# Kernel optimization log

Measured on AMD Instinct MI355X. Metric: run time of the kernel, lower is better.

The kernel has to match this reference:

```python
import jax, jax.numpy as jnp
import numpy as np

BLOCK = 32          # MX block size along the contraction dim
E4M3_MAX = 448.0    # max finite magnitude of float8_e4m3fn
E4M3_MAX_EXP = 8.0  # floor(log2(448)) = 8


def mxfp8_quant_dequant(t):
    """Simulate MXFP8 (OCP MX spec): per-32-block E8M0 power-of-two scale,
    elements cast to float8_e4m3fn, then dequantized back to fp32."""
    orig_shape = t.shape
    tb = t.reshape(-1, BLOCK)
    amax = jnp.max(jnp.abs(tb), axis=-1, keepdims=True)
    # E8M0 shared scale: 2^(floor(log2(amax)) - emax_e4m3)
    exp = jnp.floor(jnp.log2(jnp.maximum(amax, 2.0 ** -126))) - E4M3_MAX_EXP
    scale = jnp.exp2(exp)
    q = jnp.clip(tb / scale, -E4M3_MAX, E4M3_MAX)
    q = q.astype(jnp.float8_e4m3fn).astype(t.dtype)  # round-to-nearest fp8
    return (q * scale).reshape(orig_shape)


def setup_inputs() -> dict:
    key = jax.random.key(0)
    k1, k2, k3 = jax.random.split(key, 3)
    B, S, D_IN, D_OUT = 4, 4096, 4096, 4096
    x = jax.random.normal(k1, (B, S, D_IN), dtype=jnp.float32)
    weight = jax.random.normal(k2, (D_OUT, D_IN), dtype=jnp.float32) * 0.02
    bias = jax.random.normal(k3, (D_OUT,), dtype=jnp.float32) * 0.02
    return {"x": x, "weight": weight, "bias": bias}


def reference(x, weight, bias):
    B, S, D_IN = x.shape
    # Inline activation quantization to MXFP8 (blocks of 32 along in_features)
    x2 = x.reshape(-1, D_IN)                 # [B*S, D_IN]
    x_dq = mxfp8_quant_dequant(x2)
    # Weight is stored MXFP8-quantized; dequantize with its block scales
    w_dq = mxfp8_quant_dequant(weight)       # [D_OUT, D_IN]
    out = jnp.einsum('nk,ok->no', x_dq, w_dq) + bias  # microscaled GEMM
    return out.reshape(B, S, -1)
```

## Files before the change

### kernel.cpp

```cpp
#include <hip/hip_runtime.h>
#include <hip/hip_bf16.h>
#include <stdint.h>

typedef __attribute__((ext_vector_type(8))) short bf16x8;
typedef __attribute__((ext_vector_type(4))) float f32x4;
typedef __attribute__((ext_vector_type(8))) unsigned short u16x8;

#define BM 256
#define BN 256
#define BKT 64
#define ABYTES (BM * BKT * 2)
#define BBYTES (BN * BKT * 2)
#define BUFBYTES (ABYTES + BBYTES)

__device__ __forceinline__ float mx_qd_elem(float x, int e) {
    float xs = ldexpf(x, -e);
    xs = fminf(448.f, fmaxf(-448.f, xs));
    float a = fabsf(xs);
    float r;
    if (a < 0.015625f) {
        r = ldexpf(rintf(ldexpf(a, 9)), -9);
    } else {
        int E = (int)((__float_as_uint(a) >> 23) & 0xFF) - 127;
        r = ldexpf(rintf(ldexpf(a, 3 - E)), E - 3);
    }
    r = copysignf(r, xs);
    return ldexpf(r, e);
}

__global__ __launch_bounds__(256) void mx_quant_bf16(
    const float* __restrict__ in, uint16_t* __restrict__ out, int nblk) {
    int t = blockIdx.x * 256 + threadIdx.x;
    if (t >= nblk) return;
    const float4* p = (const float4*)(in + (size_t)t * 32);
    float v[32];
#pragma unroll
    for (int i = 0; i < 8; ++i) {
        float4 fv = p[i];
        v[4 * i + 0] = fv.x; v[4 * i + 1] = fv.y;
        v[4 * i + 2] = fv.z; v[4 * i + 3] = fv.w;
    }
    float amax = 0.f;
#pragma unroll
    for (int i = 0; i < 32; ++i) amax = fmaxf(amax, fabsf(v[i]));
    amax = fmaxf(amax, 1.17549435e-38f);
    int e = (int)((__float_as_uint(amax) >> 23) & 0xFF) - 127 - 8;

    unsigned short res[32];
#pragma unroll
    for (int i = 0; i < 32; ++i) {
        float d = mx_qd_elem(v[i], e);
        res[i] = (unsigned short)(__float_as_uint(d) >> 16);
    }
    u16x8* o = (u16x8*)(out + (size_t)t * 32);
#pragma unroll
    for (int j = 0; j < 4; ++j) {
        u16x8 pack;
#pragma unroll
        for (int i = 0; i < 8; ++i) pack[i] = res[8 * j + i];
        o[j] = pack;
    }
}

#define GLOAD(srcp, ldsoff)                                                     \
    __builtin_amdgcn_global_load_lds(                                           \
        (const __attribute__((address_space(1))) void*)(srcp),                  \
        (__attribute__((address_space(3))) void*)&lds[ldsoff], 16, 0, 0)

__global__ __launch_bounds__(512, 2) void gemm_256_bf16(
    const uint16_t* __restrict__ A, const uint16_t* __restrict__ B,
    const float* __restrict__ bias, float* __restrict__ C,
    int Nrows, int K, int O) {
    __shared__ __align__(16) uint8_t lds[2 * BUFBYTES];

    const int tid  = threadIdx.x;
    const int lane = tid & 63;
    const int w    = tid >> 6;
    const int f    = lane & 15, g = lane >> 4;
    const int wm   = w >> 2,    wn = w & 3;

    const int nwg  = gridDim.x * gridDim.y;
    const int flat = blockIdx.y * gridDim.x + blockIdx.x;
    const int swz  = (flat & 7) * (nwg >> 3) + (flat >> 3);
    const int bx   = swz % gridDim.x, by = swz / gridDim.x;
    const int rowBase = by * BM, colBase = bx * BN;

    const int rl   = lane >> 3;
    const int scol = ((lane & 7) * 16) ^ (rl << 4);
    const uint8_t* gA = (const uint8_t*)A;
    const uint8_t* gB = (const uint8_t*)B;
    const size_t K2 = (size_t)K * 2;

    int aoff[8][2], boff[4][2];
#pragma unroll
    for (int kk = 0; kk < 2; ++kk) {
        const int colb = (kk * 64 + g * 16) ^ ((f & 7) << 4);
#pragma unroll
        for (int m = 0; m < 8; ++m)
            aoff[m][kk] = (wm * 128 + m * 16 + f) * 128 + colb;
#pragma unroll
        for (int n = 0; n < 4; ++n)
            boff[n][kk] = ABYTES + (wn * 64 + n * 16 + f) * 128 + colb;
    }

    f32x4 acc[8][4];
#pragma unroll
    for (int m = 0; m < 8; ++m)
#pragma unroll
        for (int n = 0; n < 4; ++n)
#pragma unroll
            for (int j = 0; j < 4; ++j) acc[m][n][j] = 0.f;

    const int nt = K / BKT;

#define STAGE(t) do {                                                           \
        const int _buf = ((t) & 1) * BUFBYTES;                                  \
        const size_t _kb = (size_t)(t) * (BKT * 2);                             \
        _Pragma("unroll")                                                       \
        for (int _i = 0; _i < 4; ++_i)                                          \
            GLOAD(gA + (size_t)(rowBase + _i * 64 + w * 8 + rl) * K2 + _kb + scol, \
                  _buf + _i * 8192 + w * 1024);                                 \
        _Pragma("unroll")                                                       \
        for (int _i = 0; _i < 4; ++_i)                                          \
            GLOAD(gB + (size_t)(colBase + _i * 64 + w * 8 + rl) * K2 + _kb + scol, \
                  _buf + ABYTES + _i * 8192 + w * 1024);                        \
    } while (0)

    STAGE(0);
    asm volatile("s_waitcnt vmcnt(0)" ::: "memory");
    __builtin_amdgcn_sched_barrier(0);
    __builtin_amdgcn_s_barrier();
    __builtin_amdgcn_sched_barrier(0);

    for (int t = 0; t < nt; ++t) {
        if (t + 1 < nt) STAGE(t + 1);
        const int base = (t & 1) * BUFBYTES;

        bf16x8 bfr[4][2];
#pragma unroll
        for (int n = 0; n < 4; ++n) {
            bfr[n][0] = *(const bf16x8*)&lds[base + boff[n][0]];
            bfr[n][1] = *(const bf16x8*)&lds[base + boff[n][1]];
        }
#pragma unroll
        for (int m = 0; m < 8; ++m) {
            bf16x8 a0 = *(const bf16x8*)&lds[base + aoff[m][0]];
            bf16x8 a1 = *(const bf16x8*)&lds[base + aoff[m][1]];
            __builtin_amdgcn_s_setprio(1);
#pragma unroll
            for (int n = 0; n < 4; ++n) {
                acc[m][n] = __builtin_amdgcn_mfma_f32_16x16x32_bf16(
                    a0, bfr[n][0], acc[m][n], 0, 0, 0);
                acc[m][n] = __builtin_amdgcn_mfma_f32_16x16x32_bf16(
                    a1, bfr[n][1], acc[m][n], 0, 0, 0);
            }
            __builtin_amdgcn_s_setprio(0);
        }
        asm volatile("s_waitcnt vmcnt(0)" ::: "memory");
        __builtin_amdgcn_sched_barrier(0);
        __builtin_amdgcn_s_barrier();
        __builtin_amdgcn_sched_barrier(0);
    }
#undef STAGE

    const int qr = g * 4;
#pragma unroll
    for (int n = 0; n < 4; ++n) {
        int col = colBase + wn * 64 + n * 16 + f;
        float bv = bias[col];
#pragma unroll
        for (int m = 0; m < 8; ++m) {
            int r0 = rowBase + wm * 128 + m * 16 + qr;
#pragma unroll
            for (int j = 0; j < 4; ++j)
                C[(size_t)(r0 + j) * O + col] = acc[m][n][j] + bv;
        }
    }
}

extern "C" void kernel_launch(void* const* d_in, const int* in_sizes, int n_in,
                              void* d_out, int out_size, void* d_ws, size_t ws_size,
                              hipStream_t stream) {
    const float* x    = (const float*)d_in[0];
    const float* wgt  = (const float*)d_in[1];
    const float* bias = (const float*)d_in[2];
    float* out = (float*)d_out;

    const int D_OUT = in_sizes[2];
    const int D_IN  = in_sizes[1] / D_OUT;
    const int NROWS = in_sizes[0] / D_IN;

    uint16_t* xq = (uint16_t*)d_ws;
    uint16_t* wq = xq + (size_t)NROWS * D_IN;

    int nblkx = NROWS * (D_IN / 32);
    int nblkw = D_OUT * (D_IN / 32);
    mx_quant_bf16<<<dim3((nblkx + 255) / 256), dim3(256), 0, stream>>>(x, xq, nblkx);
    mx_quant_bf16<<<dim3((nblkw + 255) / 256), dim3(256), 0, stream>>>(wgt, wq, nblkw);

    dim3 grid(D_OUT / BN, NROWS / BM);
    gemm_256_bf16<<<grid, dim3(512), 0, stream>>>(xq, wq, bias, out,
                                                  NROWS, D_IN, D_OUT);
}
```

Measured before the change: 607.4 us.

## Split GEMM main loop into four barrier-synced phases interleaving loads and MFMAs

Restructures the bf16 GEMM main loop into four quadrant phases, modeled on an 8-wave ping-pong schedule. Each phase issues a subset of the next tile's global-to-LDS loads, reads its LDS fragments and runs a 4x2 MFMA quadrant, with partial vmcnt waits and extra barriers. Global load addressing is also precomputed per row group, with a simpler thread-to-LDS mapping. The goal is to overlap memory traffic with MFMA work and reduce register pressure from fragments, at the cost of more barriers and a more fragile wait-count ordering.

```diff
diff --git a/kernel.cpp b/kernel.cpp
--- a/kernel.cpp
+++ b/kernel.cpp
@@ -67,7 +67,7 @@
         (const __attribute__((address_space(1))) void*)(srcp),                  \
         (__attribute__((address_space(3))) void*)&lds[ldsoff], 16, 0, 0)
 
-__global__ __launch_bounds__(512, 2) void gemm_256_bf16(
+__global__ __launch_bounds__(512, 2) void gemm_8p_bf16(
     const uint16_t* __restrict__ A, const uint16_t* __restrict__ B,
     const float* __restrict__ bias, float* __restrict__ C,
     int Nrows, int K, int O) {
@@ -85,11 +85,20 @@
     const int bx   = swz % gridDim.x, by = swz / gridDim.x;
     const int rowBase = by * BM, colBase = bx * BN;
 
-    const int rl   = lane >> 3;
-    const int scol = ((lane & 7) * 16) ^ (rl << 4);
-    const uint8_t* gA = (const uint8_t*)A;
-    const uint8_t* gB = (const uint8_t*)B;
+    const int sri = tid >> 3;
+    const int ssc = ((tid & 7) * 16) ^ ((sri & 7) << 4);
+    const int sld = tid * 16;
     const size_t K2 = (size_t)K * 2;
+    const uint8_t* gAr[4]; const uint8_t* gBr[4];
+#pragma unroll
+    for (int r = 0; r < 4; ++r) {
+        gAr[r] = (const uint8_t*)A + (size_t)(rowBase + r * 64 + sri) * K2 + ssc;
+        gBr[r] = (const uint8_t*)B + (size_t)(colBase + r * 64 + sri) * K2 + ssc;
+    }
+#define SA(t, r) GLOAD(gAr[r] + (size_t)(t) * (BKT * 2),                        \
+                       (((t) & 1) * BUFBYTES) + (r) * 8192 + sld)
+#define SB(t, r) GLOAD(gBr[r] + (size_t)(t) * (BKT * 2),                        \
+                       (((t) & 1) * BUFBYTES) + ABYTES + (r) * 8192 + sld)
 
     int aoff[8][2], boff[4][2];
 #pragma unroll
@@ -113,55 +122,81 @@
 
     const int nt = K / BKT;
 
-#define STAGE(t) do {                                                           \
-        const int _buf = ((t) & 1) * BUFBYTES;                                  \
-        const size_t _kb = (size_t)(t) * (BKT * 2);                             \
-        _Pragma("unroll")                                                       \
-        for (int _i = 0; _i < 4; ++_i)                                          \
-            GLOAD(gA + (size_t)(rowBase + _i * 64 + w * 8 + rl) * K2 + _kb + scol, \
-                  _buf + _i * 8192 + w * 1024);                                 \
-        _Pragma("unroll")                                                       \
-        for (int _i = 0; _i < 4; ++_i)                                          \
-            GLOAD(gB + (size_t)(colBase + _i * 64 + w * 8 + rl) * K2 + _kb + scol, \
-                  _buf + ABYTES + _i * 8192 + w * 1024);                        \
+#define LD_A(AF, MB) do {                                                       \
+        _Pragma("unroll") for (int _m = 0; _m < 4; ++_m) {                      \
+            AF[_m][0] = *(const bf16x8*)&lds[bb + aoff[(MB) + _m][0]];          \
+            AF[_m][1] = *(const bf16x8*)&lds[bb + aoff[(MB) + _m][1]];          \
+        } } while (0)
+#define LD_B(BF, NB) do {                                                       \
+        _Pragma("unroll") for (int _n = 0; _n < 2; ++_n) {                      \
+            BF[_n][0] = *(const bf16x8*)&lds[bb + boff[(NB) + _n][0]];          \
+            BF[_n][1] = *(const bf16x8*)&lds[bb + boff[(NB) + _n][1]];          \
+        } } while (0)
+#define MFMA_Q(MB, NB, AF, BF) do {                                             \
+        __builtin_amdgcn_s_setprio(1);                                          \
+        _Pragma("unroll") for (int _m = 0; _m < 4; ++_m)                        \
+        _Pragma("unroll") for (int _n = 0; _n < 2; ++_n) {                      \
+            acc[(MB)+_m][(NB)+_n] = __builtin_amdgcn_mfma_f32_16x16x32_bf16(    \
+                AF[_m][0], BF[_n][0], acc[(MB)+_m][(NB)+_n], 0, 0, 0);          \
+            acc[(MB)+_m][(NB)+_n] = __builtin_amdgcn_mfma_f32_16x16x32_bf16(    \
+                AF[_m][1], BF[_n][1], acc[(MB)+_m][(NB)+_n], 0, 0, 0);          \
+        }                                                                       \
+        __builtin_amdgcn_s_setprio(0);                                          \
     } while (0)
-
-    STAGE(0);
-    asm volatile("s_waitcnt vmcnt(0)" ::: "memory");
+#define BAR()    __builtin_amdgcn_s_barrier()
+#define LGKM0()  do { asm volatile("s_waitcnt lgkmcnt(0)" ::: "memory");        \
+                      __builtin_amdgcn_sched_barrier(0); } while (0)
+
+    SB(0, 0); SB(0, 1); SB(0, 2); SB(0, 3);
+    SA(0, 0); SA(0, 2); SA(0, 1); SA(0, 3);
+    asm volatile("s_waitcnt vmcnt(2)" ::: "memory");
     __builtin_amdgcn_sched_barrier(0);
-    __builtin_amdgcn_s_barrier();
-    __builtin_amdgcn_sched_barrier(0);
+    BAR();
 
     for (int t = 0; t < nt; ++t) {
-        if (t + 1 < nt) STAGE(t + 1);
-        const int base = (t & 1) * BUFBYTES;
-
-        bf16x8 bfr[4][2];
-#pragma unroll
-        for (int n = 0; n < 4; ++n) {
-            bfr[n][0] = *(const bf16x8*)&lds[base + boff[n][0]];
-            bfr[n][1] = *(const bf16x8*)&lds[base + boff[n][1]];
-        }
-#pragma unroll
-        for (int m = 0; m < 8; ++m) {
-            bf16x8 a0 = *(const bf16x8*)&lds[base + aoff[m][0]];
-            bf16x8 a1 = *(const bf16x8*)&lds[base + aoff[m][1]];
-            __builtin_amdgcn_s_setprio(1);
-#pragma unroll
-            for (int n = 0; n < 4; ++n) {
-                acc[m][n] = __builtin_amdgcn_mfma_f32_16x16x32_bf16(
-                    a0, bfr[n][0], acc[m][n], 0, 0, 0);
-                acc[m][n] = __builtin_amdgcn_mfma_f32_16x16x32_bf16(
-                    a1, bfr[n][1], acc[m][n], 0, 0, 0);
-            }
-            __builtin_amdgcn_s_setprio(0);
-        }
-        asm volatile("s_waitcnt vmcnt(0)" ::: "memory");
+        const int bb = (t & 1) * BUFBYTES;
+        const bool pf = (t + 1) < nt;
+        bf16x8 afr[4][2], bfr[2][2], bfr2[2][2];
+
+        LD_A(afr, 0);
+        LD_B(bfr, 0);
+        if (pf) { SB(t + 1, 0); SB(t + 1, 1); }
+        asm volatile("s_waitcnt lgkmcnt(8)" ::: "memory");
+        BAR(); LGKM0();
+        MFMA_Q(0, 0, afr, bfr);
+        BAR();
+
+        LD_B(bfr2, 2);
+        if (pf) { SB(t + 1, 2); SB(t + 1, 3); }
+        BAR(); LGKM0();
+        MFMA_Q(0, 2, afr, bfr2);
+        if (pf) asm volatile("s_waitcnt vmcnt(4)" ::: "memory");
+        else    asm volatile("s_waitcnt vmcnt(0)" ::: "memory");
         __builtin_amdgcn_sched_barrier(0);
-        __builtin_amdgcn_s_barrier();
+        BAR();
+
+        LD_A(afr, 4);
+        if (pf) { SA(t + 1, 0); SA(t + 1, 2); }
+        BAR(); LGKM0();
+        MFMA_Q(4, 2, afr, bfr2);
+        BAR();
+
+        LD_B(bfr, 0);
+        if (pf) { SA(t + 1, 1); SA(t + 1, 3); }
+        BAR(); LGKM0();
+        MFMA_Q(4, 0, afr, bfr);
+        if (pf) asm volatile("s_waitcnt vmcnt(2)" ::: "memory");
+        else    asm volatile("s_waitcnt vmcnt(0)" ::: "memory");
         __builtin_amdgcn_sched_barrier(0);
-    }
-#undef STAGE
+        BAR();
+    }
+#undef SA
+#undef SB
+#undef LD_A
+#undef LD_B
+#undef MFMA_Q
+#undef BAR
+#undef LGKM0
 
     const int qr = g * 4;
 #pragma unroll
@@ -199,6 +234,6 @@
     mx_quant_bf16<<<dim3((nblkw + 255) / 256), dim3(256), 0, stream>>>(wgt, wq, nblkw);
 
     dim3 grid(D_OUT / BN, NROWS / BM);
-    gemm_256_bf16<<<grid, dim3(512), 0, stream>>>(xq, wq, bias, out,
-                                                  NROWS, D_IN, D_OUT);
-}
+    gemm_8p_bf16<<<grid, dim3(512), 0, stream>>>(xq, wq, bias, out,
+                                                 NROWS, D_IN, D_OUT);
+}
```

New measurement: 623.1 us. 1.03x slower.

## Interleave LDS fragment reads with MFMA groups using explicit lgkmcnt waits

Applied to the files above, without the earlier changes.

The GEMM main loop is restructured so LDS fragment reads for the second K half and upper M rows are issued while the earlier MFMA groups run. Partial lgkmcnt waits and sched barriers enforce this ordering. Global prefetch addresses are now precomputed per thread as base pointers, which cuts per-iteration address arithmetic. The aim is to hide LDS read latency behind matrix-core work, at the cost of more live fragment registers and a rigid hand schedule.

```diff
diff --git a/kernel.cpp b/kernel.cpp
--- a/kernel.cpp
+++ b/kernel.cpp
@@ -67,7 +67,7 @@
         (const __attribute__((address_space(1))) void*)(srcp),                  \
         (__attribute__((address_space(3))) void*)&lds[ldsoff], 16, 0, 0)
 
-__global__ __launch_bounds__(512, 2) void gemm_256_bf16(
+__global__ __launch_bounds__(512, 2) void gemm_ck_bf16(
     const uint16_t* __restrict__ A, const uint16_t* __restrict__ B,
     const float* __restrict__ bias, float* __restrict__ C,
     int Nrows, int K, int O) {
@@ -85,45 +85,60 @@
     const int bx   = swz % gridDim.x, by = swz / gridDim.x;
     const int rowBase = by * BM, colBase = bx * BN;
 
-    const int rl   = lane >> 3;
-    const int scol = ((lane & 7) * 16) ^ (rl << 4);
-    const uint8_t* gA = (const uint8_t*)A;
-    const uint8_t* gB = (const uint8_t*)B;
+    const int sri = tid >> 3;
+    const int ssc = ((tid & 7) * 16) ^ ((sri & 7) << 4);
+    const int sld = tid * 16;
     const size_t K2 = (size_t)K * 2;
-
-    int aoff[8][2], boff[4][2];
-#pragma unroll
-    for (int kk = 0; kk < 2; ++kk) {
-        const int colb = (kk * 64 + g * 16) ^ ((f & 7) << 4);
-#pragma unroll
-        for (int m = 0; m < 8; ++m)
-            aoff[m][kk] = (wm * 128 + m * 16 + f) * 128 + colb;
-#pragma unroll
-        for (int n = 0; n < 4; ++n)
-            boff[n][kk] = ABYTES + (wn * 64 + n * 16 + f) * 128 + colb;
-    }
-
-    f32x4 acc[8][4];
-#pragma unroll
-    for (int m = 0; m < 8; ++m)
-#pragma unroll
-        for (int n = 0; n < 4; ++n)
-#pragma unroll
-            for (int j = 0; j < 4; ++j) acc[m][n][j] = 0.f;
-
-    const int nt = K / BKT;
-
+    const uint8_t* gAr[4]; const uint8_t* gBr[4];
+#pragma unroll
+    for (int r = 0; r < 4; ++r) {
+        gAr[r] = (const uint8_t*)A + (size_t)(rowBase + r * 64 + sri) * K2 + ssc;
+        gBr[r] = (const uint8_t*)B + (size_t)(colBase + r * 64 + sri) * K2 + ssc;
+    }
 #define STAGE(t) do {                                                           \
         const int _buf = ((t) & 1) * BUFBYTES;                                  \
         const size_t _kb = (size_t)(t) * (BKT * 2);                             \
         _Pragma("unroll")                                                       \
         for (int _i = 0; _i < 4; ++_i)                                          \
-            GLOAD(gA + (size_t)(rowBase + _i * 64 + w * 8 + rl) * K2 + _kb + scol, \
-                  _buf + _i * 8192 + w * 1024);                                 \
+            GLOAD(gAr[_i] + _kb, _buf + _i * 8192 + sld);                       \
         _Pragma("unroll")                                                       \
         for (int _i = 0; _i < 4; ++_i)                                          \
-            GLOAD(gB + (size_t)(colBase + _i * 64 + w * 8 + rl) * K2 + _kb + scol, \
-                  _buf + ABYTES + _i * 8192 + w * 1024);                        \
+            GLOAD(gBr[_i] + _kb, _buf + ABYTES + _i * 8192 + sld);              \
+    } while (0)
+
+    int aoff[8][2], boff[4][2];
+#pragma unroll
+    for (int kk = 0; kk < 2; ++kk) {
+        const int colb = (kk * 64 + g * 16) ^ ((f & 7) << 4);
+#pragma unroll
+        for (int m = 0; m < 8; ++m)
+            aoff[m][kk] = (wm * 128 + m * 16 + f) * 128 + colb;
+#pragma unroll
+        for (int n = 0; n < 4; ++n)
+            boff[n][kk] = ABYTES + (wn * 64 + n * 16 + f) * 128 + colb;
+    }
+
+    f32x4 acc[8][4];
+#pragma unroll
+    for (int m = 0; m < 8; ++m)
+#pragma unroll
+        for (int n = 0; n < 4; ++n)
+#pragma unroll
+            for (int j = 0; j < 4; ++j) acc[m][n][j] = 0.f;
+
+    const int nt = K / BKT;
+
+#define WAITL(N) do {                                                           \
+        asm volatile("s_waitcnt lgkmcnt(" #N ")" ::: "memory");                 \
+        __builtin_amdgcn_sched_barrier(0);                                      \
+    } while (0)
+#define MFMA_C(MB, AF, BF) do {                                                 \
+        __builtin_amdgcn_s_setprio(1);                                          \
+        _Pragma("unroll") for (int _m = 0; _m < 4; ++_m)                        \
+        _Pragma("unroll") for (int _n = 0; _n < 4; ++_n)                        \
+            acc[(MB) + _m][_n] = __builtin_amdgcn_mfma_f32_16x16x32_bf16(       \
+                AF[_m], BF[_n], acc[(MB) + _m][_n], 0, 0, 0);                   \
+        __builtin_amdgcn_s_setprio(0);                                          \
     } while (0)
 
     STAGE(0);
@@ -133,35 +148,39 @@
     __builtin_amdgcn_sched_barrier(0);
 
     for (int t = 0; t < nt; ++t) {
-        if (t + 1 < nt) STAGE(t + 1);
-        const int base = (t & 1) * BUFBYTES;
-
-        bf16x8 bfr[4][2];
-#pragma unroll
-        for (int n = 0; n < 4; ++n) {
-            bfr[n][0] = *(const bf16x8*)&lds[base + boff[n][0]];
-            bfr[n][1] = *(const bf16x8*)&lds[base + boff[n][1]];
-        }
-#pragma unroll
-        for (int m = 0; m < 8; ++m) {
-            bf16x8 a0 = *(const bf16x8*)&lds[base + aoff[m][0]];
-            bf16x8 a1 = *(const bf16x8*)&lds[base + aoff[m][1]];
-            __builtin_amdgcn_s_setprio(1);
-#pragma unroll
-            for (int n = 0; n < 4; ++n) {
-                acc[m][n] = __builtin_amdgcn_mfma_f32_16x16x32_bf16(
-                    a0, bfr[n][0], acc[m][n], 0, 0, 0);
-                acc[m][n] = __builtin_amdgcn_mfma_f32_16x16x32_bf16(
-                    a1, bfr[n][1], acc[m][n], 0, 0, 0);
-            }
-            __builtin_amdgcn_s_setprio(0);
-        }
+        const int bb = (t & 1) * BUFBYTES;
+        const bool pf = (t + 1) < nt;
+        bf16x8 bA[4], bB[4], aLo[4], aHi[4], aLo1[4], aHi1[4];
+
+#pragma unroll
+        for (int n = 0; n < 4; ++n) bA[n] = *(const bf16x8*)&lds[bb + boff[n][0]];
+#pragma unroll
+        for (int m = 0; m < 4; ++m) aLo[m] = *(const bf16x8*)&lds[bb + aoff[m][0]];
+#pragma unroll
+        for (int m = 0; m < 4; ++m) aHi[m] = *(const bf16x8*)&lds[bb + aoff[4 + m][0]];
+        if (pf) STAGE(t + 1);
+        WAITL(4);
+        MFMA_C(0, aLo, bA);
+#pragma unroll
+        for (int n = 0; n < 4; ++n) bB[n] = *(const bf16x8*)&lds[bb + boff[n][1]];
+#pragma unroll
+        for (int m = 0; m < 4; ++m) aLo1[m] = *(const bf16x8*)&lds[bb + aoff[m][1]];
+        WAITL(8);
+        MFMA_C(4, aHi, bA);
+#pragma unroll
+        for (int m = 0; m < 4; ++m) aHi1[m] = *(const bf16x8*)&lds[bb + aoff[4 + m][1]];
+        WAITL(4);
+        MFMA_C(0, aLo1, bB);
+        WAITL(0);
+        MFMA_C(4, aHi1, bB);
         asm volatile("s_waitcnt vmcnt(0)" ::: "memory");
         __builtin_amdgcn_sched_barrier(0);
         __builtin_amdgcn_s_barrier();
         __builtin_amdgcn_sched_barrier(0);
     }
 #undef STAGE
+#undef WAITL
+#undef MFMA_C
 
     const int qr = g * 4;
 #pragma unroll
@@ -199,6 +218,6 @@
     mx_quant_bf16<<<dim3((nblkw + 255) / 256), dim3(256), 0, stream>>>(wgt, wq, nblkw);
 
     dim3 grid(D_OUT / BN, NROWS / BM);
-    gemm_256_bf16<<<grid, dim3(512), 0, stream>>>(xq, wq, bias, out,
-                                                  NROWS, D_IN, D_OUT);
-}
+    gemm_ck_bf16<<<grid, dim3(512), 0, stream>>>(xq, wq, bias, out,
+                                                 NROWS, D_IN, D_OUT);
+}
```

Measured after the change: 587.3 us. 3.3% less time.
